# Performance work log

Hardware: AMD Instinct MI355X
Metric: run time of the kernel (lower is better)

The kernel has to match this reference:

```python
import jax, jax.numpy as jnp
import numpy as np

TIME_STEP = 7


def _trilinear_sample(vol, coords):
    """3D grid_sample, mode='bilinear' (trilinear), padding_mode='border',
    align_corners=True.  vol: [B,C,D,H,W], coords: [B,D,H,W,3] with last
    axis ordered (x=w, y=h, z=d) in normalized [-1,1] coords."""
    B, C, D, H, W = vol.shape
    # unnormalize (align_corners=True) and clamp (border padding)
    x = jnp.clip((coords[..., 0] + 1.0) * 0.5 * (W - 1), 0.0, W - 1.0)
    y = jnp.clip((coords[..., 1] + 1.0) * 0.5 * (H - 1), 0.0, H - 1.0)
    z = jnp.clip((coords[..., 2] + 1.0) * 0.5 * (D - 1), 0.0, D - 1.0)

    x0f, y0f, z0f = jnp.floor(x), jnp.floor(y), jnp.floor(z)
    wx, wy, wz = x - x0f, y - y0f, z - z0f

    x0 = x0f.astype(jnp.int32)
    y0 = y0f.astype(jnp.int32)
    z0 = z0f.astype(jnp.int32)
    x1 = jnp.minimum(x0 + 1, W - 1)
    y1 = jnp.minimum(y0 + 1, H - 1)
    z1 = jnp.minimum(z0 + 1, D - 1)

    N = D * H * W
    vol_f = vol.reshape(B, C, N)

    def gather(zi, yi, xi):
        idx = ((zi * H + yi) * W + xi).reshape(B, 1, N)
        return jnp.take_along_axis(vol_f, jnp.broadcast_to(idx, (B, C, N)), axis=2)

    wx_ = wx.reshape(B, 1, N)
    wy_ = wy.reshape(B, 1, N)
    wz_ = wz.reshape(B, 1, N)

    out = (gather(z0, y0, x0) * (1 - wz_) * (1 - wy_) * (1 - wx_)
         + gather(z0, y0, x1) * (1 - wz_) * (1 - wy_) * wx_
         + gather(z0, y1, x0) * (1 - wz_) * wy_ * (1 - wx_)
         + gather(z0, y1, x1) * (1 - wz_) * wy_ * wx_
         + gather(z1, y0, x0) * wz_ * (1 - wy_) * (1 - wx_)
         + gather(z1, y0, x1) * wz_ * (1 - wy_) * wx_
         + gather(z1, y1, x0) * wz_ * wy_ * (1 - wx_)
         + gather(z1, y1, x1) * wz_ * wy_ * wx_)
    return out.reshape(B, C, D, H, W)


def setup_inputs() -> dict:
    key = jax.random.key(0)
    flow = jax.random.normal(key, (1, 3, 160, 192, 160), dtype=jnp.float32)
    return {"flow": flow}


def reference(flow):
    B, C, D, H, W = flow.shape
    gd, gh, gw = jnp.meshgrid(jnp.linspace(-1.0, 1.0, D),
                              jnp.linspace(-1.0, 1.0, H),
                              jnp.linspace(-1.0, 1.0, W), indexing='ij')
    # grid_sample coord order is (x=w, y=h, z=d)
    base_grid = jnp.stack([gw, gh, gd], axis=-1).astype(flow.dtype)  # [D,H,W,3]

    flow = flow / (2 ** TIME_STEP)

    def step(f, _):
        # deformation = stack(grid_w+flow_w, grid_h+flow_h, grid_d+flow_d)
        disp = jnp.stack([f[:, 2], f[:, 1], f[:, 0]], axis=-1)  # [B,D,H,W,3]
        coords = base_grid[None] + disp
        f = f + _trilinear_sample(f, coords)
        return f, None

    flow, _ = jax.lax.scan(step, flow, None, length=TIME_STEP)
    return flow
```

## Files before the change

kernel.cpp:

```cpp
#include <hip/hip_runtime.h>


#define DD 160
#define HH 192
#define WW 160
#define NVOX (DD * HH * WW)
#define NBLK (NVOX / 256)

template<bool IN_PACKED, bool OUT_PACKED>
__global__ __launch_bounds__(256) void diffeo_step_t(const float* __restrict__ in,
                                                     float* __restrict__ out,
                                                     float scale) {
    const int b = blockIdx.x;
    const int l = (b & 7) * (NBLK / 8) + (b >> 3);
    const int tid = l * 256 + (int)threadIdx.x;

    const int w = tid % WW;
    const int t = tid / WW;
    const int h = t % HH;
    const int d = t / HH;

    float f0, f1, f2;
    if (IN_PACKED) {
        const float* p = in + 3 * tid;
        f0 = p[0]; f1 = p[1]; f2 = p[2];
    } else {
        f0 = in[tid] * scale;
        f1 = in[NVOX + tid] * scale;
        f2 = in[2 * NVOX + tid] * scale;
    }

    const float gx = -1.0f + 2.0f * (float)w / (float)(WW - 1);
    const float gy = -1.0f + 2.0f * (float)h / (float)(HH - 1);
    const float gz = -1.0f + 2.0f * (float)d / (float)(DD - 1);
    float x = (gx + f2 + 1.0f) * (0.5f * (float)(WW - 1));
    float y = (gy + f1 + 1.0f) * (0.5f * (float)(HH - 1));
    float z = (gz + f0 + 1.0f) * (0.5f * (float)(DD - 1));
    x = fminf(fmaxf(x, 0.0f), (float)(WW - 1));
    y = fminf(fmaxf(y, 0.0f), (float)(HH - 1));
    z = fminf(fmaxf(z, 0.0f), (float)(DD - 1));

    const float x0f = floorf(x), y0f = floorf(y), z0f = floorf(z);
    const float wx = x - x0f, wy = y - y0f, wz = z - z0f;
    const int x0 = (int)x0f, y0 = (int)y0f, z0 = (int)z0f;
    const int x1 = min(x0 + 1, WW - 1);
    const int y1 = min(y0 + 1, HH - 1);
    const int z1 = min(z0 + 1, DD - 1);

    const int b00 = (z0 * HH + y0) * WW;
    const int b01 = (z0 * HH + y1) * WW;
    const int b10 = (z1 * HH + y0) * WW;
    const int b11 = (z1 * HH + y1) * WW;
    const int i000 = b00 + x0, i001 = b00 + x1;
    const int i010 = b01 + x0, i011 = b01 + x1;
    const int i100 = b10 + x0, i101 = b10 + x1;
    const int i110 = b11 + x0, i111 = b11 + x1;

    const float omx = 1.0f - wx, omy = 1.0f - wy, omz = 1.0f - wz;
    const float w000 = omz * omy * omx, w001 = omz * omy * wx;
    const float w010 = omz * wy * omx,  w011 = omz * wy * wx;
    const float w100 = wz * omy * omx,  w101 = wz * omy * wx;
    const float w110 = wz * wy * omx,   w111 = wz * wy * wx;

    float s0, s1, s2;
    if (IN_PACKED) {
        const float* p000 = in + 3 * i000;  const float* p001 = in + 3 * i001;
        const float* p010 = in + 3 * i010;  const float* p011 = in + 3 * i011;
        const float* p100 = in + 3 * i100;  const float* p101 = in + 3 * i101;
        const float* p110 = in + 3 * i110;  const float* p111 = in + 3 * i111;
        const float a0 = p000[0], a1 = p000[1], a2 = p000[2];
        const float b0_ = p001[0], b1_ = p001[1], b2_ = p001[2];
        const float c0 = p010[0], c1 = p010[1], c2 = p010[2];
        const float e0 = p011[0], e1 = p011[1], e2 = p011[2];
        const float g0 = p100[0], g1 = p100[1], g2 = p100[2];
        const float h0 = p101[0], h1 = p101[1], h2 = p101[2];
        const float j0 = p110[0], j1 = p110[1], j2 = p110[2];
        const float k0 = p111[0], k1 = p111[1], k2 = p111[2];
        s0 = a0*w000 + b0_*w001 + c0*w010 + e0*w011 + g0*w100 + h0*w101 + j0*w110 + k0*w111;
        s1 = a1*w000 + b1_*w001 + c1*w010 + e1*w011 + g1*w100 + h1*w101 + j1*w110 + k1*w111;
        s2 = a2*w000 + b2_*w001 + c2*w010 + e2*w011 + g2*w100 + h2*w101 + j2*w110 + k2*w111;
    } else {
        const float* v0 = in;
        const float* v1 = in + NVOX;
        const float* v2 = in + 2 * NVOX;
        const float a000 = v0[i000], a001 = v0[i001], a010 = v0[i010], a011 = v0[i011];
        const float a100 = v0[i100], a101 = v0[i101], a110 = v0[i110], a111 = v0[i111];
        const float b000 = v1[i000], b001 = v1[i001], b010 = v1[i010], b011 = v1[i011];
        const float b100 = v1[i100], b101 = v1[i101], b110 = v1[i110], b111 = v1[i111];
        const float c000 = v2[i000], c001 = v2[i001], c010 = v2[i010], c011 = v2[i011];
        const float c100 = v2[i100], c101 = v2[i101], c110 = v2[i110], c111 = v2[i111];
        s0 = (a000*w000 + a001*w001 + a010*w010 + a011*w011
            + a100*w100 + a101*w101 + a110*w110 + a111*w111) * scale;
        s1 = (b000*w000 + b001*w001 + b010*w010 + b011*w011
            + b100*w100 + b101*w101 + b110*w110 + b111*w111) * scale;
        s2 = (c000*w000 + c001*w001 + c010*w010 + c011*w011
            + c100*w100 + c101*w101 + c110*w110 + c111*w111) * scale;
    }

    const float r0 = f0 + s0;
    const float r1 = f1 + s1;
    const float r2 = f2 + s2;

    if (OUT_PACKED) {
        float* q = out + 3 * tid;
        q[0] = r0; q[1] = r1; q[2] = r2;
    } else {
        out[tid]            = r0;
        out[NVOX + tid]     = r1;
        out[2 * NVOX + tid] = r2;
    }
}

extern "C" void kernel_launch(void* const* d_in, const int* in_sizes, int n_in,
                              void* d_out, int out_size, void* d_ws, size_t ws_size,
                              hipStream_t stream) {
    const float* flow = (const float*)d_in[0];
    float* out = (float*)d_out;
    float* ws  = (float*)d_ws;

    const float inv128 = 1.0f / 128.0f;

    diffeo_step_t<false, true><<<NBLK, 256, 0, stream>>>(flow, out, inv128);
    diffeo_step_t<true,  true><<<NBLK, 256, 0, stream>>>(out, ws, 1.0f);
    diffeo_step_t<true,  true><<<NBLK, 256, 0, stream>>>(ws, out, 1.0f);
    diffeo_step_t<true,  true><<<NBLK, 256, 0, stream>>>(out, ws, 1.0f);
    diffeo_step_t<true,  true><<<NBLK, 256, 0, stream>>>(ws, out, 1.0f);
    diffeo_step_t<true,  true><<<NBLK, 256, 0, stream>>>(out, ws, 1.0f);
    diffeo_step_t<true, false><<<NBLK, 256, 0, stream>>>(ws, out, 1.0f);
}
```

Measured before the change: 601.7 us.

## Switch intermediate flow layout to padded float4 for vectorized corner gathers

Adds a separate pack kernel that converts the planar input into a padded float4 (xyz plus zero) interleaved buffer. All seven integration steps then gather each trilinear corner with a single 16-byte load instead of three scalar loads. The final step writes planar output. This costs one extra launch and about a third more memory traffic per voxel for the padding, and it needs two float4 workspace buffers; when the workspace is too small it falls back to a packed-3 path, which also uses the extra pack kernel.

```diff
diff --git a/kernel.cpp b/kernel.cpp
--- a/kernel.cpp
+++ b/kernel.cpp
@@ -7,28 +7,42 @@
 #define NVOX (DD * HH * WW)
 #define NBLK (NVOX / 256)
 
-template<bool IN_PACKED, bool OUT_PACKED>
-__global__ __launch_bounds__(256) void diffeo_step_t(const float* __restrict__ in,
-                                                     float* __restrict__ out,
-                                                     float scale) {
+__device__ __forceinline__ int swizzled_tid() {
     const int b = blockIdx.x;
     const int l = (b & 7) * (NBLK / 8) + (b >> 3);
-    const int tid = l * 256 + (int)threadIdx.x;
+    return l * 256 + (int)threadIdx.x;
+}
 
+__global__ __launch_bounds__(256) void pack4_kernel(const float* __restrict__ in,
+                                                    float4* __restrict__ out, float scale) {
+    const int tid = blockIdx.x * 256 + (int)threadIdx.x;
+    float4 v;
+    v.x = in[tid] * scale;
+    v.y = in[NVOX + tid] * scale;
+    v.z = in[2 * NVOX + tid] * scale;
+    v.w = 0.0f;
+    out[tid] = v;
+}
+
+__global__ __launch_bounds__(256) void pack3_kernel(const float* __restrict__ in,
+                                                    float* __restrict__ out, float scale) {
+    const int tid = blockIdx.x * 256 + (int)threadIdx.x;
+    float* q = out + 3 * tid;
+    q[0] = in[tid] * scale;
+    q[1] = in[NVOX + tid] * scale;
+    q[2] = in[2 * NVOX + tid] * scale;
+}
+
+struct Corners {
+    int i000, i001, i010, i011, i100, i101, i110, i111;
+    float w000, w001, w010, w011, w100, w101, w110, w111;
+};
+
+__device__ __forceinline__ Corners make_corners(int tid, float f0, float f1, float f2) {
     const int w = tid % WW;
     const int t = tid / WW;
     const int h = t % HH;
     const int d = t / HH;
-
-    float f0, f1, f2;
-    if (IN_PACKED) {
-        const float* p = in + 3 * tid;
-        f0 = p[0]; f1 = p[1]; f2 = p[2];
-    } else {
-        f0 = in[tid] * scale;
-        f1 = in[NVOX + tid] * scale;
-        f2 = in[2 * NVOX + tid] * scale;
-    }
 
     const float gx = -1.0f + 2.0f * (float)w / (float)(WW - 1);
     const float gy = -1.0f + 2.0f * (float)h / (float)(HH - 1);
@@ -51,63 +65,87 @@
     const int b01 = (z0 * HH + y1) * WW;
     const int b10 = (z1 * HH + y0) * WW;
     const int b11 = (z1 * HH + y1) * WW;
-    const int i000 = b00 + x0, i001 = b00 + x1;
-    const int i010 = b01 + x0, i011 = b01 + x1;
-    const int i100 = b10 + x0, i101 = b10 + x1;
-    const int i110 = b11 + x0, i111 = b11 + x1;
+
+    Corners c;
+    c.i000 = b00 + x0; c.i001 = b00 + x1;
+    c.i010 = b01 + x0; c.i011 = b01 + x1;
+    c.i100 = b10 + x0; c.i101 = b10 + x1;
+    c.i110 = b11 + x0; c.i111 = b11 + x1;
 
     const float omx = 1.0f - wx, omy = 1.0f - wy, omz = 1.0f - wz;
-    const float w000 = omz * omy * omx, w001 = omz * omy * wx;
-    const float w010 = omz * wy * omx,  w011 = omz * wy * wx;
-    const float w100 = wz * omy * omx,  w101 = wz * omy * wx;
-    const float w110 = wz * wy * omx,   w111 = wz * wy * wx;
+    c.w000 = omz * omy * omx; c.w001 = omz * omy * wx;
+    c.w010 = omz * wy * omx;  c.w011 = omz * wy * wx;
+    c.w100 = wz * omy * omx;  c.w101 = wz * omy * wx;
+    c.w110 = wz * wy * omx;   c.w111 = wz * wy * wx;
+    return c;
+}
 
-    float s0, s1, s2;
-    if (IN_PACKED) {
-        const float* p000 = in + 3 * i000;  const float* p001 = in + 3 * i001;
-        const float* p010 = in + 3 * i010;  const float* p011 = in + 3 * i011;
-        const float* p100 = in + 3 * i100;  const float* p101 = in + 3 * i101;
-        const float* p110 = in + 3 * i110;  const float* p111 = in + 3 * i111;
-        const float a0 = p000[0], a1 = p000[1], a2 = p000[2];
-        const float b0_ = p001[0], b1_ = p001[1], b2_ = p001[2];
-        const float c0 = p010[0], c1 = p010[1], c2 = p010[2];
-        const float e0 = p011[0], e1 = p011[1], e2 = p011[2];
-        const float g0 = p100[0], g1 = p100[1], g2 = p100[2];
-        const float h0 = p101[0], h1 = p101[1], h2 = p101[2];
-        const float j0 = p110[0], j1 = p110[1], j2 = p110[2];
-        const float k0 = p111[0], k1 = p111[1], k2 = p111[2];
-        s0 = a0*w000 + b0_*w001 + c0*w010 + e0*w011 + g0*w100 + h0*w101 + j0*w110 + k0*w111;
-        s1 = a1*w000 + b1_*w001 + c1*w010 + e1*w011 + g1*w100 + h1*w101 + j1*w110 + k1*w111;
-        s2 = a2*w000 + b2_*w001 + c2*w010 + e2*w011 + g2*w100 + h2*w101 + j2*w110 + k2*w111;
-    } else {
-        const float* v0 = in;
-        const float* v1 = in + NVOX;
-        const float* v2 = in + 2 * NVOX;
-        const float a000 = v0[i000], a001 = v0[i001], a010 = v0[i010], a011 = v0[i011];
-        const float a100 = v0[i100], a101 = v0[i101], a110 = v0[i110], a111 = v0[i111];
-        const float b000 = v1[i000], b001 = v1[i001], b010 = v1[i010], b011 = v1[i011];
-        const float b100 = v1[i100], b101 = v1[i101], b110 = v1[i110], b111 = v1[i111];
-        const float c000 = v2[i000], c001 = v2[i001], c010 = v2[i010], c011 = v2[i011];
-        const float c100 = v2[i100], c101 = v2[i101], c110 = v2[i110], c111 = v2[i111];
-        s0 = (a000*w000 + a001*w001 + a010*w010 + a011*w011
-            + a100*w100 + a101*w101 + a110*w110 + a111*w111) * scale;
-        s1 = (b000*w000 + b001*w001 + b010*w010 + b011*w011
-            + b100*w100 + b101*w101 + b110*w110 + b111*w111) * scale;
-        s2 = (c000*w000 + c001*w001 + c010*w010 + c011*w011
-            + c100*w100 + c101*w101 + c110*w110 + c111*w111) * scale;
-    }
+template<bool OUT_PLANAR>
+__global__ __launch_bounds__(256) void step4_kernel(const float4* __restrict__ in,
+                                                    float* __restrict__ out) {
+    const int tid = swizzled_tid();
+    const float4 f = in[tid];
+    const Corners c = make_corners(tid, f.x, f.y, f.z);
 
-    const float r0 = f0 + s0;
-    const float r1 = f1 + s1;
-    const float r2 = f2 + s2;
+    const float4 q000 = in[c.i000], q001 = in[c.i001];
+    const float4 q010 = in[c.i010], q011 = in[c.i011];
+    const float4 q100 = in[c.i100], q101 = in[c.i101];
+    const float4 q110 = in[c.i110], q111 = in[c.i111];
 
-    if (OUT_PACKED) {
-        float* q = out + 3 * tid;
-        q[0] = r0; q[1] = r1; q[2] = r2;
-    } else {
+    const float s0 = q000.x*c.w000 + q001.x*c.w001 + q010.x*c.w010 + q011.x*c.w011
+                   + q100.x*c.w100 + q101.x*c.w101 + q110.x*c.w110 + q111.x*c.w111;
+    const float s1 = q000.y*c.w000 + q001.y*c.w001 + q010.y*c.w010 + q011.y*c.w011
+                   + q100.y*c.w100 + q101.y*c.w101 + q110.y*c.w110 + q111.y*c.w111;
+    const float s2 = q000.z*c.w000 + q001.z*c.w001 + q010.z*c.w010 + q011.z*c.w011
+                   + q100.z*c.w100 + q101.z*c.w101 + q110.z*c.w110 + q111.z*c.w111;
+
+    const float r0 = f.x + s0, r1 = f.y + s1, r2 = f.z + s2;
+    if (OUT_PLANAR) {
         out[tid]            = r0;
         out[NVOX + tid]     = r1;
         out[2 * NVOX + tid] = r2;
+    } else {
+        float4 v; v.x = r0; v.y = r1; v.z = r2; v.w = 0.0f;
+        ((float4*)out)[tid] = v;
+    }
+}
+
+template<bool OUT_PLANAR>
+__global__ __launch_bounds__(256) void step3_kernel(const float* __restrict__ in,
+                                                    float* __restrict__ out) {
+    const int tid = swizzled_tid();
+    const float* p = in + 3 * tid;
+    const float f0 = p[0], f1 = p[1], f2 = p[2];
+    const Corners c = make_corners(tid, f0, f1, f2);
+
+    const float* p000 = in + 3 * c.i000;  const float* p001 = in + 3 * c.i001;
+    const float* p010 = in + 3 * c.i010;  const float* p011 = in + 3 * c.i011;
+    const float* p100 = in + 3 * c.i100;  const float* p101 = in + 3 * c.i101;
+    const float* p110 = in + 3 * c.i110;  const float* p111 = in + 3 * c.i111;
+    const float a0 = p000[0], a1 = p000[1], a2 = p000[2];
+    const float b0 = p001[0], b1 = p001[1], b2 = p001[2];
+    const float c0 = p010[0], c1 = p010[1], c2 = p010[2];
+    const float e0 = p011[0], e1 = p011[1], e2 = p011[2];
+    const float g0 = p100[0], g1 = p100[1], g2 = p100[2];
+    const float h0 = p101[0], h1 = p101[1], h2 = p101[2];
+    const float j0 = p110[0], j1 = p110[1], j2 = p110[2];
+    const float k0 = p111[0], k1 = p111[1], k2 = p111[2];
+
+    const float s0 = a0*c.w000 + b0*c.w001 + c0*c.w010 + e0*c.w011
+                   + g0*c.w100 + h0*c.w101 + j0*c.w110 + k0*c.w111;
+    const float s1 = a1*c.w000 + b1*c.w001 + c1*c.w010 + e1*c.w011
+                   + g1*c.w100 + h1*c.w101 + j1*c.w110 + k1*c.w111;
+    const float s2 = a2*c.w000 + b2*c.w001 + c2*c.w010 + e2*c.w011
+                   + g2*c.w100 + h2*c.w101 + j2*c.w110 + k2*c.w111;
+
+    const float r0 = f0 + s0, r1 = f1 + s1, r2 = f2 + s2;
+    if (OUT_PLANAR) {
+        out[tid]            = r0;
+        out[NVOX + tid]     = r1;
+        out[2 * NVOX + tid] = r2;
+    } else {
+        float* q = out + 3 * tid;
+        q[0] = r0; q[1] = r1; q[2] = r2;
     }
 }
 
@@ -116,15 +154,29 @@
                               hipStream_t stream) {
     const float* flow = (const float*)d_in[0];
     float* out = (float*)d_out;
-    float* ws  = (float*)d_ws;
-
     const float inv128 = 1.0f / 128.0f;
 
-    diffeo_step_t<false, true><<<NBLK, 256, 0, stream>>>(flow, out, inv128);
-    diffeo_step_t<true,  true><<<NBLK, 256, 0, stream>>>(out, ws, 1.0f);
-    diffeo_step_t<true,  true><<<NBLK, 256, 0, stream>>>(ws, out, 1.0f);
-    diffeo_step_t<true,  true><<<NBLK, 256, 0, stream>>>(out, ws, 1.0f);
-    diffeo_step_t<true,  true><<<NBLK, 256, 0, stream>>>(ws, out, 1.0f);
-    diffeo_step_t<true,  true><<<NBLK, 256, 0, stream>>>(out, ws, 1.0f);
-    diffeo_step_t<true, false><<<NBLK, 256, 0, stream>>>(ws, out, 1.0f);
+    const size_t need4 = 2ull * NVOX * sizeof(float4);
+    if (ws_size >= need4) {
+        float4* A = (float4*)d_ws;
+        float4* B = A + NVOX;
+        pack4_kernel<<<NBLK, 256, 0, stream>>>(flow, A, inv128);
+        step4_kernel<false><<<NBLK, 256, 0, stream>>>(A, (float*)B);
+        step4_kernel<false><<<NBLK, 256, 0, stream>>>(B, (float*)A);
+        step4_kernel<false><<<NBLK, 256, 0, stream>>>(A, (float*)B);
+        step4_kernel<false><<<NBLK, 256, 0, stream>>>(B, (float*)A);
+        step4_kernel<false><<<NBLK, 256, 0, stream>>>(A, (float*)B);
+        step4_kernel<false><<<NBLK, 256, 0, stream>>>(B, (float*)A);
+        step4_kernel<true ><<<NBLK, 256, 0, stream>>>(A, out);
+    } else {
+        float* ws = (float*)d_ws;
+        pack3_kernel<<<NBLK, 256, 0, stream>>>(flow, ws, inv128);
+        step3_kernel<false><<<NBLK, 256, 0, stream>>>(ws, out);
+        step3_kernel<false><<<NBLK, 256, 0, stream>>>(out, ws);
+        step3_kernel<false><<<NBLK, 256, 0, stream>>>(ws, out);
+        step3_kernel<false><<<NBLK, 256, 0, stream>>>(out, ws);
+        step3_kernel<false><<<NBLK, 256, 0, stream>>>(ws, out);
+        step3_kernel<false><<<NBLK, 256, 0, stream>>>(out, ws);
+        step3_kernel<true ><<<NBLK, 256, 0, stream>>>(ws, out);
+    }
 }
```

Measured after the change: 647.6 us. +7.6%, slower.
